# Kernel tuning notes

Measured on AMD Instinct MI355X. Metric: run time of the kernel, lower is better.

## Reference

```python
import jax, jax.numpy as jnp
import numpy as np

B, D, OUT = 256, 63, 128
DP = D + 1  # 64


def setup_inputs() -> dict:
    key = jax.random.key(0)
    k1, k2, k3, k4, k5 = jax.random.split(key, 5)
    return {
        "x": jax.random.normal(k1, (B, D), dtype=jnp.float32),
        "protein_output": jax.random.normal(k2, (B, D), dtype=jnp.float32),
        "dynamic_output": jax.random.normal(k3, (B, D), dtype=jnp.float32),
        "W": jax.random.normal(k4, (DP ** 3, OUT), dtype=jnp.float32) * 0.02,
        "b": jax.random.normal(k5, (OUT,), dtype=jnp.float32) * 0.02,
    }


def reference(x, protein_output, dynamic_output, W, b):
    bsz = x.shape[0]
    ones = jnp.ones((bsz, 1), dtype=x.dtype)
    a = jnp.concatenate([x, ones], axis=1)               # [B, D+1]
    p = jnp.concatenate([protein_output, ones], axis=1)   # [B, D+1]
    d = jnp.concatenate([dynamic_output, ones], axis=1)   # [B, D+1]
    # rank-1 trilinear outer product, flattened row-major: idx = (i*(D+1)+j)*(D+1)+k
    ab = jnp.einsum('bi,bj->bij', a, p)                   # [B, D+1, D+1]
    abc = jnp.einsum('bij,bk->bijk', ab, d)               # [B, D+1, D+1, D+1]
    feat = abc.reshape(bsz, -1)                           # [B, (D+1)^3]
    return feat @ W + b                                   # [B, OUT]
```

## Files before the change

### kernel.cpp

```cpp
#include <hip/hip_runtime.h>
#include <hip/hip_bf16.h>

typedef __attribute__((ext_vector_type(8))) short short8v;
typedef __attribute__((ext_vector_type(4))) float floatx4;

__device__ __forceinline__ unsigned int pkbf(float a, float b) {
  __hip_bfloat162 h = __float22bfloat162_rn(make_float2(a, b));
  union { __hip_bfloat162 h; unsigned int u; } c; c.h = h;
  return c.u;
}

__global__ void bias_init(const float* __restrict__ bias, float* __restrict__ out) {
  int idx = blockIdx.x * 256 + threadIdx.x;
  out[idx] = bias[idx & 127];
}

__global__ __launch_bounds__(512)
void reduce_v5(const float* __restrict__ part, const float* __restrict__ bias,
               float* __restrict__ out) {
  const int tid = threadIdx.x;
  const int col = tid & 127;
  const int qr = tid >> 7;
  const int b = blockIdx.x;

  const float* pp = part + (long)qr * 16 * 32768 + (long)(col >> 5) * 8192
                    + b * 32 + (col & 31);
  float s0 = 0.f, s1 = 0.f, s2 = 0.f, s3 = 0.f;
  #pragma unroll
  for (int n = 0; n < 16; n += 4) {
    s0 += __builtin_nontemporal_load(pp + (long)n * 32768);
    s1 += __builtin_nontemporal_load(pp + (long)(n + 1) * 32768);
    s2 += __builtin_nontemporal_load(pp + (long)(n + 2) * 32768);
    s3 += __builtin_nontemporal_load(pp + (long)(n + 3) * 32768);
  }
  float sum = (s0 + s1) + (s2 + s3);

  __shared__ float red[3][128];
  if (qr) red[qr - 1][col] = sum;
  __syncthreads();
  if (qr == 0)
    out[b * 128 + col] = sum + red[0][col] + red[1][col] + red[2][col] + bias[col];
}

__global__ __launch_bounds__(512, 2)
void tfn_gemm_v5(const float* __restrict__ X, const float* __restrict__ P,
                 const float* __restrict__ Dyn, const float* __restrict__ W,
                 float* __restrict__ part) {
  __shared__ __align__(16) float wt[2][64 * 33];
  __shared__ float p_lds[64][257];

  const int tid = threadIdx.x;
  const int wv = tid >> 6, lane = tid & 63;
  const int q = lane >> 4, l16 = lane & 15;

  const int bx = blockIdx.x;
  const int ig = bx >> 2;
  const int cq = bx & 3;

  const int lrow = tid >> 3, lc4 = tid & 7;
  const float* wsrc = W + ((long)ig << 19) + (cq << 5) + lrow * 128 + (lc4 << 2);

  floatx4 rg = __builtin_nontemporal_load((const floatx4*)wsrc);

  #pragma unroll 4
  for (int k = 0; k < 32; ++k) {
    int idx = tid + (k << 9);
    if (idx < 16128) {
      int bb = idx / 63;
      int jj = idx - bb * 63;
      p_lds[jj][bb] = P[idx];
    }
  }
  if (tid < 256) p_lds[63][tid] = 1.0f;

  float e[2][2][8];
  #pragma unroll
  for (int rt = 0; rt < 2; ++rt) {
    int brow = (wv << 5) + (rt << 4) + l16;
    float av = (ig < 63) ? X[brow * 63 + ig] : 1.0f;
    #pragma unroll
    for (int h = 0; h < 2; ++h) {
      int kb = (h << 5) + (q << 3);
      #pragma unroll
      for (int t = 0; t < 8; ++t) {
        int k = kb + t;
        float dv = (k < 63) ? Dyn[brow * 63 + k] : 1.0f;
        e[rt][h][t] = av * dv;
      }
    }
  }

  floatx4 acc[2][2];
  #pragma unroll
  for (int a = 0; a < 2; ++a)
    #pragma unroll
    for (int b = 0; b < 2; ++b) acc[a][b] = (floatx4)0.0f;

  {
    float* wd = &wt[0][lrow * 33 + (lc4 << 2)];
    wd[0] = rg.x; wd[1] = rg.y; wd[2] = rg.z; wd[3] = rg.w;
  }
  rg = __builtin_nontemporal_load((const floatx4*)(wsrc + (1 << 13)));

  const int wrb = (q << 3) * 33 + l16;
  const int prow = (wv << 5) + l16;

  __syncthreads();

  for (int j = 0; j < 64; ++j) {
    float pbv[2];
    pbv[0] = p_lds[j][prow];
    pbv[1] = p_lds[j][prow + 16];

    if (j < 63) {
      float* wd = &wt[(j + 1) & 1][lrow * 33 + (lc4 << 2)];
      wd[0] = rg.x; wd[1] = rg.y; wd[2] = rg.z; wd[3] = rg.w;
      if (j < 62)
        rg = __builtin_nontemporal_load((const floatx4*)(wsrc + ((long)(j + 2) << 13)));
    }

    const float* wcur = wt[j & 1];
    #pragma unroll
    for (int h = 0; h < 2; ++h) {
      float w[2][8];
      #pragma unroll
      for (int nt = 0; nt < 2; ++nt)
        #pragma unroll
        for (int t = 0; t < 8; ++t)
          w[nt][t] = wcur[wrb + h * 1056 + t * 33 + (nt << 4)];

      union { short8v v; unsigned int u[4]; } fb[2], fa[2];
      #pragma unroll
      for (int nt = 0; nt < 2; ++nt)
        #pragma unroll
        for (int v2 = 0; v2 < 4; ++v2)
          fb[nt].u[v2] = pkbf(w[nt][2 * v2], w[nt][2 * v2 + 1]);
      #pragma unroll
      for (int rt = 0; rt < 2; ++rt)
        #pragma unroll
        for (int v2 = 0; v2 < 4; ++v2)
          fa[rt].u[v2] = pkbf(pbv[rt] * e[rt][h][2 * v2],
                              pbv[rt] * e[rt][h][2 * v2 + 1]);
      #pragma unroll
      for (int rt = 0; rt < 2; ++rt)
        #pragma unroll
        for (int nt = 0; nt < 2; ++nt)
          acc[rt][nt] = __builtin_amdgcn_mfma_f32_16x16x32_bf16(
              fa[rt].v, fb[nt].v, acc[rt][nt], 0, 0, 0);
    }
    __syncthreads();
  }

  float* pt = part + ((long)bx << 13);
  #pragma unroll
  for (int rt = 0; rt < 2; ++rt)
    #pragma unroll
    for (int nt = 0; nt < 2; ++nt) {
      int cl = (nt << 4) + l16;
      #pragma unroll
      for (int g = 0; g < 4; ++g) {
        int row = (wv << 5) + (rt << 4) + (q << 2) + g;
        pt[row * 32 + cl] = acc[rt][nt][g];
      }
    }
}

__global__ __launch_bounds__(512, 2)
void tfn_gemm(const float* __restrict__ X, const float* __restrict__ P,
              const float* __restrict__ Dyn, const float* __restrict__ W,
              float* __restrict__ out) {
  __shared__ float p_lds[16][256];

  const int tid = threadIdx.x;
  const int wv = tid >> 6, lane = tid & 63;
  const int q = lane >> 4, l16 = lane & 15;
  const int r = wv & 3;
  const int cg = wv >> 2;

  const int c = blockIdx.x;
  const int i = c >> 2;
  const int j0 = (c & 3) << 4;
  const long gk0 = (long)c << 10;

  for (int idx = tid; idx < 256 * 16; idx += 512) {
    int bb = idx >> 4, jj = idx & 15;
    int j = j0 + jj;
    p_lds[jj][bb] = (j < 63) ? P[bb * 63 + j] : 1.0f;
  }

  float e[4][2][8];
  #pragma unroll
  for (int rt = 0; rt < 4; ++rt) {
    int brow = (r << 6) + (rt << 4) + l16;
    float av = (i < 63) ? X[brow * 63 + i] : 1.0f;
    #pragma unroll
    for (int h = 0; h < 2; ++h) {
      int kb = (h << 5) + (q << 3);
      #pragma unroll
      for (int t = 0; t < 8; ++t) {
        int k = kb + t;
        float dv = (k < 63) ? Dyn[brow * 63 + k] : 1.0f;
        e[rt][h][t] = av * dv;
      }
    }
  }

  floatx4 acc[4][4];
  #pragma unroll
  for (int a = 0; a < 4; ++a)
    #pragma unroll
    for (int b = 0; b < 4; ++b) acc[a][b] = (floatx4)0.0f;

  __syncthreads();

  const float* wstep = W + (gk0 + (q << 3)) * 128 + (cg << 6) + l16;

  float wA[4][8], wB[4][8];
  #pragma unroll
  for (int nt = 0; nt < 4; ++nt)
    #pragma unroll
    for (int t = 0; t < 8; ++t)
      wA[nt][t] = wstep[t * 128 + nt * 16];

  for (int jj = 0; jj < 16; ++jj) {
    float pb[4];
    #pragma unroll
    for (int rt = 0; rt < 4; ++rt)
      pb[rt] = p_lds[jj][(r << 6) + (rt << 4) + l16];

    {
      const float* wp = wstep + ((long)(2 * jj + 1) << 12);
      #pragma unroll
      for (int nt = 0; nt < 4; ++nt)
        #pragma unroll
        for (int t = 0; t < 8; ++t)
          wB[nt][t] = wp[t * 128 + nt * 16];

      union { short8v v; unsigned int u[4]; } fb[4], fa[4];
      #pragma unroll
      for (int nt = 0; nt < 4; ++nt)
        #pragma unroll
        for (int v2 = 0; v2 < 4; ++v2)
          fb[nt].u[v2] = pkbf(wA[nt][2 * v2], wA[nt][2 * v2 + 1]);
      #pragma unroll
      for (int rt = 0; rt < 4; ++rt)
        #pragma unroll
        for (int v2 = 0; v2 < 4; ++v2)
          fa[rt].u[v2] = pkbf(pb[rt] * e[rt][0][2 * v2], pb[rt] * e[rt][0][2 * v2 + 1]);
      #pragma unroll
      for (int rt = 0; rt < 4; ++rt)
        #pragma unroll
        for (int nt = 0; nt < 4; ++nt)
          acc[rt][nt] = __builtin_amdgcn_mfma_f32_16x16x32_bf16(
              fa[rt].v, fb[nt].v, acc[rt][nt], 0, 0, 0);
    }

    {
      if (jj < 15) {
        const float* wp = wstep + ((long)(2 * jj + 2) << 12);
        #pragma unroll
        for (int nt = 0; nt < 4; ++nt)
          #pragma unroll
          for (int t = 0; t < 8; ++t)
            wA[nt][t] = wp[t * 128 + nt * 16];
      }

      union { short8v v; unsigned int u[4]; } fb[4], fa[4];
      #pragma unroll
      for (int nt = 0; nt < 4; ++nt)
        #pragma unroll
        for (int v2 = 0; v2 < 4; ++v2)
          fb[nt].u[v2] = pkbf(wB[nt][2 * v2], wB[nt][2 * v2 + 1]);
      #pragma unroll
      for (int rt = 0; rt < 4; ++rt)
        #pragma unroll
        for (int v2 = 0; v2 < 4; ++v2)
          fa[rt].u[v2] = pkbf(pb[rt] * e[rt][1][2 * v2], pb[rt] * e[rt][1][2 * v2 + 1]);
      #pragma unroll
      for (int rt = 0; rt < 4; ++rt)
        #pragma unroll
        for (int nt = 0; nt < 4; ++nt)
          acc[rt][nt] = __builtin_amdgcn_mfma_f32_16x16x32_bf16(
              fa[rt].v, fb[nt].v, acc[rt][nt], 0, 0, 0);
    }
  }

  #pragma unroll
  for (int rt = 0; rt < 4; ++rt)
    #pragma unroll
    for (int nt = 0; nt < 4; ++nt) {
      int col = (cg << 6) + (nt << 4) + l16;
      #pragma unroll
      for (int g = 0; g < 4; ++g) {
        int brow = (r << 6) + (rt << 4) + (q << 2) + g;
        atomicAdd(&out[brow * 128 + col], acc[rt][nt][g]);
      }
    }
}

extern "C" void kernel_launch(void* const* d_in, const int* in_sizes, int n_in,
                              void* d_out, int out_size, void* d_ws, size_t ws_size,
                              hipStream_t stream) {
  const float* x   = (const float*)d_in[0];
  const float* p   = (const float*)d_in[1];
  const float* dyn = (const float*)d_in[2];
  const float* W   = (const float*)d_in[3];
  const float* b   = (const float*)d_in[4];
  float* out = (float*)d_out;

  const size_t part_bytes = (size_t)256 * 8192 * sizeof(float);

  if (d_ws != nullptr && ws_size >= part_bytes) {
    float* part = (float*)d_ws;
    tfn_gemm_v5<<<256, 512, 0, stream>>>(x, p, dyn, W, part);
    reduce_v5<<<256, 512, 0, stream>>>(part, b, out);
  } else {
    bias_init<<<128, 256, 0, stream>>>(b, out);
    tfn_gemm<<<256, 512, 0, stream>>>(x, p, dyn, W, out);
  }
}
```

Baseline: 237.4 us.

## Split j range across twice as many blocks with bf16-packed swizzled W staging

New measurement: 210.4 us. 1.13x faster.

```diff
diff --git a/kernel.cpp b/kernel.cpp
--- a/kernel.cpp
+++ b/kernel.cpp
@@ -3,6 +3,9 @@
 
 typedef __attribute__((ext_vector_type(8))) short short8v;
 typedef __attribute__((ext_vector_type(4))) float floatx4;
+typedef __attribute__((ext_vector_type(4))) unsigned int uint4v;
+
+union FragU { uint4v u4; unsigned int u[4]; short8v v; };
 
 __device__ __forceinline__ unsigned int pkbf(float a, float b) {
   __hip_bfloat162 h = __float22bfloat162_rn(make_float2(a, b));
@@ -16,18 +19,18 @@
 }
 
 __global__ __launch_bounds__(512)
-void reduce_v5(const float* __restrict__ part, const float* __restrict__ bias,
+void reduce_v6(const float* __restrict__ part, const float* __restrict__ bias,
                float* __restrict__ out) {
   const int tid = threadIdx.x;
   const int col = tid & 127;
   const int qr = tid >> 7;
   const int b = blockIdx.x;
 
-  const float* pp = part + (long)qr * 16 * 32768 + (long)(col >> 5) * 8192
+  const float* pp = part + (long)(qr * 128 + (col >> 5)) * 8192
                     + b * 32 + (col & 31);
   float s0 = 0.f, s1 = 0.f, s2 = 0.f, s3 = 0.f;
-  #pragma unroll
-  for (int n = 0; n < 16; n += 4) {
+  #pragma unroll 4
+  for (int n = 0; n < 32; n += 4) {
     s0 += __builtin_nontemporal_load(pp + (long)n * 32768);
     s1 += __builtin_nontemporal_load(pp + (long)(n + 1) * 32768);
     s2 += __builtin_nontemporal_load(pp + (long)(n + 2) * 32768);
@@ -42,36 +45,36 @@
     out[b * 128 + col] = sum + red[0][col] + red[1][col] + red[2][col] + bias[col];
 }
 
-__global__ __launch_bounds__(512, 2)
-void tfn_gemm_v5(const float* __restrict__ X, const float* __restrict__ P,
+__global__ __launch_bounds__(512, 4)
+void tfn_gemm_v6(const float* __restrict__ X, const float* __restrict__ P,
                  const float* __restrict__ Dyn, const float* __restrict__ W,
                  float* __restrict__ part) {
-  __shared__ __align__(16) float wt[2][64 * 33];
-  __shared__ float p_lds[64][257];
+  __shared__ unsigned int wlds[4][1024];
+  __shared__ float p_lds[32][257];
 
   const int tid = threadIdx.x;
   const int wv = tid >> 6, lane = tid & 63;
   const int q = lane >> 4, l16 = lane & 15;
 
   const int bx = blockIdx.x;
-  const int ig = bx >> 2;
+  const int ig = bx >> 3;
+  const int jh = (bx >> 2) & 1;
   const int cq = bx & 3;
 
-  const int lrow = tid >> 3, lc4 = tid & 7;
-  const float* wsrc = W + ((long)ig << 19) + (cq << 5) + lrow * 128 + (lc4 << 2);
-
-  floatx4 rg = __builtin_nontemporal_load((const floatx4*)wsrc);
-
-  #pragma unroll 4
-  for (int k = 0; k < 32; ++k) {
-    int idx = tid + (k << 9);
-    if (idx < 16128) {
-      int bb = idx / 63;
-      int jj = idx - bb * 63;
-      p_lds[jj][bb] = P[idx];
-    }
-  }
-  if (tid < 256) p_lds[63][tid] = 1.0f;
+  const int pr = tid >> 3, cc = tid & 7;
+  const float* wbase = W + ((long)ig << 19) + ((long)jh << 18)
+                       + (cq << 5) + (cc << 2) + (long)pr * 256;
+
+  floatx4 rg0 = __builtin_nontemporal_load((const floatx4*)wbase);
+  floatx4 rg1 = __builtin_nontemporal_load((const floatx4*)(wbase + 128));
+
+  #pragma unroll
+  for (int it = 0; it < 16; ++it) {
+    int idx = tid + (it << 9);
+    int jj = idx & 31, bb = idx >> 5;
+    int j = (jh << 5) + jj;
+    p_lds[jj][bb] = (j < 63) ? P[bb * 63 + j] : 1.0f;
+  }
 
   float e[2][2][8];
   #pragma unroll
@@ -90,65 +93,82 @@
     }
   }
 
+  const int wtile0 = pr >> 5;
+  const int wpr = pr & 31;
+  const int wcol = cc << 2;
+
+  {
+    unsigned int* tb = &wlds[wtile0][0];
+    #pragma unroll
+    for (int w = 0; w < 4; ++w) {
+      int col = wcol + w;
+      tb[((col << 5) + wpr) ^ ((col & 7) << 2)] = pkbf(rg0[w], rg1[w]);
+    }
+  }
+  rg0 = __builtin_nontemporal_load((const floatx4*)(wbase + (1 << 14)));
+  rg1 = __builtin_nontemporal_load((const floatx4*)(wbase + (1 << 14) + 128));
+
+  int roff[2][2];
+  #pragma unroll
+  for (int nt = 0; nt < 2; ++nt) {
+    int col = (nt << 4) + l16;
+    #pragma unroll
+    for (int h = 0; h < 2; ++h)
+      roff[nt][h] = (col << 5) + (((h << 4) + (q << 2)) ^ ((col & 7) << 2));
+  }
+  const int prow = (wv << 5) + l16;
+
   floatx4 acc[2][2];
   #pragma unroll
   for (int a = 0; a < 2; ++a)
     #pragma unroll
     for (int b = 0; b < 2; ++b) acc[a][b] = (floatx4)0.0f;
 
-  {
-    float* wd = &wt[0][lrow * 33 + (lc4 << 2)];
-    wd[0] = rg.x; wd[1] = rg.y; wd[2] = rg.z; wd[3] = rg.w;
-  }
-  rg = __builtin_nontemporal_load((const floatx4*)(wsrc + (1 << 13)));
-
-  const int wrb = (q << 3) * 33 + l16;
-  const int prow = (wv << 5) + l16;
-
   __syncthreads();
 
-  for (int j = 0; j < 64; ++j) {
-    float pbv[2];
-    pbv[0] = p_lds[j][prow];
-    pbv[1] = p_lds[j][prow + 16];
-
-    if (j < 63) {
-      float* wd = &wt[(j + 1) & 1][lrow * 33 + (lc4 << 2)];
-      wd[0] = rg.x; wd[1] = rg.y; wd[2] = rg.z; wd[3] = rg.w;
-      if (j < 62)
-        rg = __builtin_nontemporal_load((const floatx4*)(wsrc + ((long)(j + 2) << 13)));
-    }
-
-    const float* wcur = wt[j & 1];
-    #pragma unroll
-    for (int h = 0; h < 2; ++h) {
-      float w[2][8];
-      #pragma unroll
-      for (int nt = 0; nt < 2; ++nt)
-        #pragma unroll
-        for (int t = 0; t < 8; ++t)
-          w[nt][t] = wcur[wrb + h * 1056 + t * 33 + (nt << 4)];
-
-      union { short8v v; unsigned int u[4]; } fb[2], fa[2];
-      #pragma unroll
-      for (int nt = 0; nt < 2; ++nt)
-        #pragma unroll
-        for (int v2 = 0; v2 < 4; ++v2)
-          fb[nt].u[v2] = pkbf(w[nt][2 * v2], w[nt][2 * v2 + 1]);
-      #pragma unroll
-      for (int rt = 0; rt < 2; ++rt)
-        #pragma unroll
-        for (int v2 = 0; v2 < 4; ++v2)
-          fa[rt].u[v2] = pkbf(pbv[rt] * e[rt][h][2 * v2],
-                              pbv[rt] * e[rt][h][2 * v2 + 1]);
-      #pragma unroll
-      for (int rt = 0; rt < 2; ++rt)
+  for (int dt = 0; dt < 16; ++dt) {
+    if (dt < 15) {
+      unsigned int* tb = &wlds[(((dt + 1) & 1) << 1) + wtile0][0];
+      #pragma unroll
+      for (int w = 0; w < 4; ++w) {
+        int col = wcol + w;
+        tb[((col << 5) + wpr) ^ ((col & 7) << 2)] = pkbf(rg0[w], rg1[w]);
+      }
+      if (dt < 14) {
+        rg0 = __builtin_nontemporal_load((const floatx4*)(wbase + ((long)(dt + 2) << 14)));
+        rg1 = __builtin_nontemporal_load((const floatx4*)(wbase + ((long)(dt + 2) << 14) + 128));
+      }
+    }
+
+    #pragma unroll
+    for (int jj2 = 0; jj2 < 2; ++jj2) {
+      int jl = (dt << 1) + jj2;
+      const unsigned int* tb = &wlds[((dt & 1) << 1) + jj2][0];
+      float pbv[2];
+      pbv[0] = p_lds[jl][prow];
+      pbv[1] = p_lds[jl][prow + 16];
+
+      #pragma unroll
+      for (int h = 0; h < 2; ++h) {
+        FragU fb[2], fa[2];
         #pragma unroll
         for (int nt = 0; nt < 2; ++nt)
-          acc[rt][nt] = __builtin_amdgcn_mfma_f32_16x16x32_bf16(
-              fa[rt].v, fb[nt].v, acc[rt][nt], 0, 0, 0);
-    }
-    __syncthreads();
+          fb[nt].u4 = *(const uint4v*)(tb + roff[nt][h]);
+        #pragma unroll
+        for (int rt = 0; rt < 2; ++rt)
+          #pragma unroll
+          for (int v2 = 0; v2 < 4; ++v2)
+            fa[rt].u[v2] = pkbf(pbv[rt] * e[rt][h][2 * v2],
+                                pbv[rt] * e[rt][h][2 * v2 + 1]);
+        #pragma unroll
+        for (int rt = 0; rt < 2; ++rt)
+          #pragma unroll
+          for (int nt = 0; nt < 2; ++nt)
+            acc[rt][nt] = __builtin_amdgcn_mfma_f32_16x16x32_bf16(
+                fa[rt].v, fb[nt].v, acc[rt][nt], 0, 0, 0);
+      }
+    }
+    if (dt < 15) __syncthreads();
   }
 
   float* pt = part + ((long)bx << 13);
@@ -308,12 +328,12 @@
   const float* b   = (const float*)d_in[4];
   float* out = (float*)d_out;
 
-  const size_t part_bytes = (size_t)256 * 8192 * sizeof(float);
+  const size_t part_bytes = (size_t)512 * 8192 * sizeof(float);
 
   if (d_ws != nullptr && ws_size >= part_bytes) {
     float* part = (float*)d_ws;
-    tfn_gemm_v5<<<256, 512, 0, stream>>>(x, p, dyn, W, part);
-    reduce_v5<<<256, 512, 0, stream>>>(part, b, out);
+    tfn_gemm_v6<<<512, 512, 0, stream>>>(x, p, dyn, W, part);
+    reduce_v6<<<256, 512, 0, stream>>>(part, b, out);
   } else {
     bias_init<<<128, 256, 0, stream>>>(b, out);
     tfn_gemm<<<256, 512, 0, stream>>>(x, p, dyn, W, out);
```
